# Optimization experiments

Measured on AMD Instinct MI355X. Metric: run time of the kernel, lower is better.

## Reference

```python
import jax, jax.numpy as jnp
import numpy as np

EMBED_DIM, NUM_HEADS, LOCAL_SIZE = 256, 4, 15
HEAD_DIM = EMBED_DIM // NUM_HEADS
SCALING = float(HEAD_DIM) ** -0.5


def get_overlap_segments(x, window_size):
    # x: (n, t, d) -> (n, t, window_size, d), zero-padded local windows centered at each position
    n, t, d = x.shape
    p = (window_size - 1) // 2
    xp = jnp.pad(x, ((0, 0), (p, p), (0, 0)))
    idx = jnp.arange(t)[:, None] + jnp.arange(window_size)[None, :]  # (t, w)
    return xp[:, idx]


def setup_inputs():
    key = jax.random.key(0)
    ks = jax.random.split(key, 4)
    B, W, F = 4, 64, 4096
    T = W + F
    x = jax.random.normal(ks[0], (B, T, EMBED_DIM), dtype=jnp.float32)
    # block one-hot frame->window assignment (each window owns F//W consecutive frames)
    assign = jnp.repeat(jnp.arange(W), F // W)
    wm = jnp.broadcast_to(jax.nn.one_hot(assign, W, dtype=jnp.float32).T[None], (B, W, F))
    W_qkv = jax.random.normal(ks[1], (EMBED_DIM, 3 * EMBED_DIM), jnp.float32) * 0.02
    b_qkv = jnp.zeros((3 * EMBED_DIM,), jnp.float32)
    W_out = jax.random.normal(ks[2], (EMBED_DIM, EMBED_DIM), jnp.float32) * 0.02
    b_out = jnp.zeros((EMBED_DIM,), jnp.float32)
    return {"x": x, "window_mapping": wm, "W_qkv": W_qkv, "b_qkv": b_qkv,
            "W_out": W_out, "b_out": b_out}


def _to_heads(z, b, t):
    # (b, t, E) -> (b*H, t, d), matching torch transpose/reshape ordering (b outer, h inner)
    return z.reshape(b, t, NUM_HEADS, HEAD_DIM).transpose(0, 2, 1, 3).reshape(b * NUM_HEADS, t, HEAD_DIM)


def reference(x, window_mapping, W_qkv, b_qkv, W_out, b_out):
    b, t, e = x.shape
    Wn, Fn = window_mapping.shape[1], window_mapping.shape[2]
    qkv = x @ W_qkv + b_qkv
    Q, K, V = jnp.split(qkv, 3, axis=-1)
    Q = Q * SCALING
    wtok = _to_heads(x[:, :Wn], b, Wn)            # (n, W, d) raw word tokens
    Qh = _to_heads(Q, b, t)[:, Wn:]               # (n, F, d)
    Kh = _to_heads(K, b, t)[:, Wn:]
    Vh = _to_heads(V, b, t)[:, Wn:]
    wm = jnp.broadcast_to(window_mapping[:, None], (b, NUM_HEADS, Wn, Fn)).reshape(b * NUM_HEADS, Wn, Fn)
    # scatter each window's word token to its frames
    expa = jnp.einsum('nwd,nwf->nfd', wtok, wm)   # (n, F, d)
    Kseg = get_overlap_segments(Kh, LOCAL_SIZE)   # (n, F, w, d)
    Vseg = get_overlap_segments(Vh, LOCAL_SIZE)
    Kcat = jnp.concatenate([expa[:, :, None], Kseg], axis=2)  # (n, F, 1+w, d)
    scores = jnp.einsum('nfd,nfwd->nfw', Qh, Kcat)            # (n, F, 1+w)
    # word-token weight: softmax across frames within each window chunk (F % W == 0, no pad)
    chunk = Fn // Wn
    w_wtok = jax.nn.softmax(scores[:, :, 0].reshape(-1, Wn, chunk), axis=-1).reshape(-1, Fn)
    # local-window weights: softmax over the window axis
    w_fea = jax.nn.softmax(scores[:, :, 1:], axis=-1)
    attn = jnp.concatenate([w_wtok[:, :, None], w_fea], axis=2)  # (n, F, 1+w)
    Vcat = jnp.concatenate([expa[:, :, None], Vseg], axis=2)
    out_fea = jnp.einsum('nfw,nfwd->nfd', attn, Vcat)            # (n, F, d)
    out = jnp.concatenate([wtok, out_fea], axis=1)               # (n, T, d)
    out = out.reshape(b, NUM_HEADS, t, HEAD_DIM).transpose(0, 2, 1, 3).reshape(b, t, e)
    return out @ W_out + b_out
```

## Files before the change

kernel.cpp:

```cpp
#include <hip/hip_runtime.h>


#define QN 4194304ull

typedef _Float16 h8 __attribute__((ext_vector_type(8)));
typedef _Float16 h4 __attribute__((ext_vector_type(4)));
typedef float f32x16 __attribute__((ext_vector_type(16)));

__global__ __launch_bounds__(256) void conv_small(
    const float* __restrict__ x, const float* __restrict__ wm,
    const float* __restrict__ Wq, const float* __restrict__ Wo,
    _Float16* __restrict__ wqth, _Float16* __restrict__ woth,
    _Float16* __restrict__ wmth, _Float16* __restrict__ xth) {
  __shared__ float S[64 * 65];
  const int g = blockIdx.x, tid = threadIdx.x;
  if (g < 768) {
    int o = g * 256 + tid;
    int n = o >> 8, k = o & 255;
    wqth[o] = (_Float16)Wq[(size_t)k * 768 + n];
  } else if (g < 1024) {
    int o = (g - 768) * 256 + tid;
    int n = o >> 8, k = o & 255;
    woth[o] = (_Float16)Wo[(size_t)k * 256 + n];
  } else if (g < 1280) {
    int local = g - 1024;
    int b = local >> 6, f0 = (local & 63) * 64;
    {
      int w = tid >> 2, c0 = (tid & 3) * 16;
      const float* src = wm + ((size_t)(b * 64 + w)) * 4096 + f0 + c0;
#pragma unroll
      for (int cc = 0; cc < 16; cc += 4)
        *(float4*)&S[w * 65 + c0 + cc] = *(const float4*)(src + cc);
    }
    __syncthreads();
    {
      int fl = tid >> 2, w0 = (tid & 3) * 16;
      int f = f0 + fl;
      _Float16 hh[16];
#pragma unroll
      for (int j = 0; j < 16; ++j) hh[j] = (_Float16)S[(w0 + j) * 65 + fl];
      size_t o = ((size_t)b * 4096 + f) * 64 + w0;
      *(float4*)(wmth + o) = *(float4*)&hh[0];
      *(float4*)(wmth + o + 8) = *(float4*)&hh[8];
    }
  } else {
    int b = g - 1280;
    for (int c0 = 0; c0 < 256; c0 += 64) {
      __syncthreads();
      {
        int w = tid >> 2, cl0 = (tid & 3) * 16;
        const float* src = x + ((size_t)(b * 4160 + w)) * 256 + c0 + cl0;
#pragma unroll
        for (int cc = 0; cc < 16; cc += 4)
          *(float4*)&S[w * 65 + cl0 + cc] = *(const float4*)(src + cc);
      }
      __syncthreads();
      {
        int cl = tid >> 2, w0 = (tid & 3) * 16;
        _Float16 hh[16];
#pragma unroll
        for (int j = 0; j < 16; ++j) hh[j] = (_Float16)S[(w0 + j) * 65 + cl];
        size_t o = ((size_t)(b * 256 + c0 + cl)) * 64 + w0;
        *(float4*)(xth + o) = *(float4*)&hh[0];
        *(float4*)(xth + o + 8) = *(float4*)&hh[8];
      }
    }
  }
}

__global__ __launch_bounds__(256) void qkv_mfma(
    const float* __restrict__ x, const _Float16* __restrict__ wth,
    const float* __restrict__ bq,
    _Float16* __restrict__ Qh, _Float16* __restrict__ Kh,
    _Float16* __restrict__ Vh) {
  __shared__ _Float16 Ah[128][40], Bh[128][40];
  const int tid = threadIdx.x;
  const int wave = tid >> 6, lane = tid & 63;
  const int ln = lane & 31, half = lane >> 5;
  const int mw = (wave & 1) * 64, nw = (wave >> 1) * 64;
  const int m0 = blockIdx.x * 128, n0 = blockIdx.y * 128;

  const int sr = tid >> 1, scq = (tid & 1) * 16;
  const int am = m0 + sr;
  const size_t arow =
      ((size_t)((am >> 12) * 4160 + 64 + (am & 4095))) * 256 + scq;
  const size_t brow = (size_t)(n0 + sr) * 256 + scq;

  float4 rah0, rah1, rbh0, rbh1;
  auto QLOAD = [&](int k0_) {
    float4 fx0 = *(const float4*)(x + arow + k0_);
    float4 fx1 = *(const float4*)(x + arow + k0_ + 4);
    float4 fx2 = *(const float4*)(x + arow + k0_ + 8);
    float4 fx3 = *(const float4*)(x + arow + k0_ + 12);
    rbh0 = *(const float4*)(wth + brow + k0_);
    rbh1 = *(const float4*)(wth + brow + k0_ + 8);
    _Float16 hh[16] = {
        (_Float16)fx0.x, (_Float16)fx0.y, (_Float16)fx0.z, (_Float16)fx0.w,
        (_Float16)fx1.x, (_Float16)fx1.y, (_Float16)fx1.z, (_Float16)fx1.w,
        (_Float16)fx2.x, (_Float16)fx2.y, (_Float16)fx2.z, (_Float16)fx2.w,
        (_Float16)fx3.x, (_Float16)fx3.y, (_Float16)fx3.z, (_Float16)fx3.w};
    rah0 = *(float4*)&hh[0];
    rah1 = *(float4*)&hh[8];
  };

  QLOAD(0);
  f32x16 acc[2][2] = {};

  for (int it = 0; it < 8; ++it) {
    __syncthreads();
    *(float4*)&Ah[sr][scq] = rah0;
    *(float4*)&Ah[sr][scq + 8] = rah1;
    *(float4*)&Bh[sr][scq] = rbh0;
    *(float4*)&Bh[sr][scq + 8] = rbh1;
    __syncthreads();
    if (it < 7) QLOAD((it + 1) * 32);
#pragma unroll
    for (int ks = 0; ks < 2; ++ks) {
      const int kc = ks * 16 + half * 8;
      h8 a0 = *(const h8*)&Ah[mw + ln][kc];
      h8 a1 = *(const h8*)&Ah[mw + 32 + ln][kc];
      h8 b0 = *(const h8*)&Bh[nw + ln][kc];
      h8 b1 = *(const h8*)&Bh[nw + 32 + ln][kc];
      acc[0][0] = __builtin_amdgcn_mfma_f32_32x32x16_f16(a0, b0, acc[0][0], 0, 0, 0);
      acc[0][1] = __builtin_amdgcn_mfma_f32_32x32x16_f16(a0, b1, acc[0][1], 0, 0, 0);
      acc[1][0] = __builtin_amdgcn_mfma_f32_32x32x16_f16(a1, b0, acc[1][0], 0, 0, 0);
      acc[1][1] = __builtin_amdgcn_mfma_f32_32x32x16_f16(a1, b1, acc[1][1], 0, 0, 0);
    }
  }

#pragma unroll
  for (int ni = 0; ni < 2; ++ni) {
    const int c = n0 + nw + ni * 32 + ln;
    const int which = c >> 8, e = c & 255;
    const int h = e >> 6, d = e & 63;
    _Float16* dst = (which == 0) ? Qh : (which == 1) ? Kh : Vh;
    const float sc2 = (which == 0) ? 0.125f : 1.0f;
    const float bias = bq[c];
#pragma unroll
    for (int mi = 0; mi < 2; ++mi) {
      const int rb = m0 + mw + mi * 32 + 4 * half;
#pragma unroll
      for (int reg = 0; reg < 16; ++reg) {
        int rr = rb + (reg & 3) + 8 * (reg >> 2);
        int b2 = rr >> 12, f2 = rr & 4095;
        dst[(((size_t)(b2 * 4 + h)) * 4096 + f2) * 64 + d] =
            (_Float16)((acc[mi][ni][reg] + bias) * sc2);
      }
    }
  }
}

__global__ __launch_bounds__(256) void attn_fused(
    const _Float16* __restrict__ Qh, const _Float16* __restrict__ Kh,
    const _Float16* __restrict__ Vh,
    const _Float16* __restrict__ wmth, const _Float16* __restrict__ xth,
    _Float16* __restrict__ OFh) {
  __shared__ float Ks[78][68];
  __shared__ float Vs[78][68];
  __shared__ float EXs[64][68];
  __shared__ float s0s[64];
  __shared__ float red[2];
  const int tid = threadIdx.x;
  const int w = blockIdx.x;
  const int n = blockIdx.y;
  const int f0 = w * 64;
  const int b = n >> 2, h = n & 3;

  for (int idx = tid; idx < 78 * 16; idx += 256) {
    int rr = idx >> 4, c = (idx & 15) * 4;
    int g = f0 - 7 + rr;
    float4 kv = {0.f, 0.f, 0.f, 0.f}, vv = {0.f, 0.f, 0.f, 0.f};
    if (g >= 0 && g < 4096) {
      size_t base = ((size_t)n * 4096 + g) * 64 + c;
      h4 k4 = *(const h4*)(Kh + base);
      h4 v4 = *(const h4*)(Vh + base);
      kv = {(float)k4.x, (float)k4.y, (float)k4.z, (float)k4.w};
      vv = {(float)v4.x, (float)v4.y, (float)v4.z, (float)v4.w};
    }
    *(float4*)&Ks[rr][c] = kv;
    *(float4*)&Vs[rr][c] = vv;
  }
  {
    const int wave = tid >> 6, lane = tid & 63;
    const int ln = lane & 31, half = lane >> 5;
    const int mi = wave & 1, ni = wave >> 1;
    const size_t arow = ((size_t)(b * 4096 + f0 + mi * 32 + ln)) * 64 + half * 8;
    const size_t brow =
        ((size_t)(b * 256 + h * 64 + ni * 32 + ln)) * 64 + half * 8;
    f32x16 eacc = {};
#pragma unroll
    for (int ks = 0; ks < 4; ++ks) {
      const int kc = ks * 16;
      h8 ah = *(const h8*)(wmth + arow + kc);
      h8 bh = *(const h8*)(xth + brow + kc);
      eacc = __builtin_amdgcn_mfma_f32_32x32x16_f16(ah, bh, eacc, 0, 0, 0);
    }
    const int col = ni * 32 + ln;
    const int rb2 = mi * 32 + 4 * half;
#pragma unroll
    for (int reg = 0; reg < 16; ++reg)
      EXs[rb2 + (reg & 3) + 8 * (reg >> 2)][col] = eacc[reg];
  }
  __syncthreads();

  const int i = tid >> 2, q = tid & 3;
  const int f = f0 + i;
  const size_t qbase = ((size_t)n * 4096 + f) * 64 + q * 16;
  h8 qh0 = *(const h8*)(Qh + qbase);
  h8 qh1 = *(const h8*)(Qh + qbase + 8);
  float4 q0 = {(float)qh0.s0, (float)qh0.s1, (float)qh0.s2, (float)qh0.s3};
  float4 q1 = {(float)qh0.s4, (float)qh0.s5, (float)qh0.s6, (float)qh0.s7};
  float4 q2 = {(float)qh1.s0, (float)qh1.s1, (float)qh1.s2, (float)qh1.s3};
  float4 q3 = {(float)qh1.s4, (float)qh1.s5, (float)qh1.s6, (float)qh1.s7};
  float4 e0 = *(const float4*)&EXs[i][q * 16];
  float4 e1 = *(const float4*)&EXs[i][q * 16 + 4];
  float4 e2 = *(const float4*)&EXs[i][q * 16 + 8];
  float4 e3 = *(const float4*)&EXs[i][q * 16 + 12];

  float s0 = q0.x * e0.x + q0.y * e0.y + q0.z * e0.z + q0.w * e0.w +
             q1.x * e1.x + q1.y * e1.y + q1.z * e1.z + q1.w * e1.w +
             q2.x * e2.x + q2.y * e2.y + q2.z * e2.z + q2.w * e2.w +
             q3.x * e3.x + q3.y * e3.y + q3.z * e3.z + q3.w * e3.w;
  s0 += __shfl_xor(s0, 1);
  s0 += __shfl_xor(s0, 2);

  float sj[15];
#pragma unroll
  for (int j = 0; j < 15; ++j) {
    const float* kr = &Ks[i + j][q * 16];
    float4 k0 = *(const float4*)(kr);
    float4 k1 = *(const float4*)(kr + 4);
    float4 k2 = *(const float4*)(kr + 8);
    float4 k3 = *(const float4*)(kr + 12);
    float s = q0.x * k0.x + q0.y * k0.y + q0.z * k0.z + q0.w * k0.w +
              q1.x * k1.x + q1.y * k1.y + q1.z * k1.z + q1.w * k1.w +
              q2.x * k2.x + q2.y * k2.y + q2.z * k2.z + q2.w * k2.w +
              q3.x * k3.x + q3.y * k3.y + q3.z * k3.z + q3.w * k3.w;
    s += __shfl_xor(s, 1);
    s += __shfl_xor(s, 2);
    sj[j] = s;
  }

  if (q == 0) s0s[i] = s0;
  __syncthreads();
  if (tid < 64) {
    float v = s0s[tid];
    float m = v;
    for (int o = 1; o < 64; o <<= 1) m = fmaxf(m, __shfl_xor(m, o));
    float ee = expf(v - m);
    float s = ee;
    for (int o = 1; o < 64; o <<= 1) s += __shfl_xor(s, o);
    if (tid == 0) { red[0] = m; red[1] = s; }
  }
  __syncthreads();
  const float wt = expf(s0 - red[0]) / red[1];

  float mx = sj[0];
#pragma unroll
  for (int j = 1; j < 15; ++j) mx = fmaxf(mx, sj[j]);
  float pj[15], den = 0.f;
#pragma unroll
  for (int j = 0; j < 15; ++j) { pj[j] = expf(sj[j] - mx); den += pj[j]; }
  const float inv = 1.0f / den;

  float o[16] = {wt * e0.x, wt * e0.y, wt * e0.z, wt * e0.w,
                 wt * e1.x, wt * e1.y, wt * e1.z, wt * e1.w,
                 wt * e2.x, wt * e2.y, wt * e2.z, wt * e2.w,
                 wt * e3.x, wt * e3.y, wt * e3.z, wt * e3.w};
#pragma unroll
  for (int j = 0; j < 15; ++j) {
    float wj = pj[j] * inv;
    const float* vr = &Vs[i + j][q * 16];
#pragma unroll
    for (int dd = 0; dd < 16; ++dd) o[dd] = fmaf(wj, vr[dd], o[dd]);
  }
  _Float16 oh[16];
#pragma unroll
  for (int dd = 0; dd < 16; ++dd) oh[dd] = (_Float16)o[dd];
  *(float4*)(OFh + qbase) = *(float4*)&oh[0];
  *(float4*)(OFh + qbase + 8) = *(float4*)&oh[8];
}

__global__ __launch_bounds__(256) void out_mfma(
    const float* __restrict__ x, const _Float16* __restrict__ ofh,
    const _Float16* __restrict__ wth, const float* __restrict__ bo,
    float* __restrict__ out) {
  __shared__ _Float16 Ah[64][72], Bh[64][72];
  const int tid = threadIdx.x;
  const int wave = tid >> 6, lane = tid & 63;
  const int ln = lane & 31, half = lane >> 5;
  const int mw = (wave & 1) * 32, nw = (wave >> 1) * 32;
  const int m0 = blockIdx.x * 64, n0 = blockIdx.y * 64;
  const int sr = tid >> 2, sc4 = (tid & 3) * 16;
  const int m = m0 + sr;
  const int b = m / 4160, tt = m % 4160;
  const bool useX = (tt < 64);
  const size_t xrow = ((size_t)(b * 4160 + tt)) * 256 + sc4;
  const long obase = ((long)(b * 4) * 4096 + (tt - 64)) * 64 + sc4;
  const size_t bbase = (size_t)(n0 + sr) * 256 + sc4;

  float4 ra0, ra1, rb0, rb1;
  auto OLOAD = [&](int k0_) {
    if (useX) {
      float4 fx0 = *(const float4*)(x + xrow + k0_);
      float4 fx1 = *(const float4*)(x + xrow + k0_ + 4);
      float4 fx2 = *(const float4*)(x + xrow + k0_ + 8);
      float4 fx3 = *(const float4*)(x + xrow + k0_ + 12);
      _Float16 hh[16] = {
          (_Float16)fx0.x, (_Float16)fx0.y, (_Float16)fx0.z, (_Float16)fx0.w,
          (_Float16)fx1.x, (_Float16)fx1.y, (_Float16)fx1.z, (_Float16)fx1.w,
          (_Float16)fx2.x, (_Float16)fx2.y, (_Float16)fx2.z, (_Float16)fx2.w,
          (_Float16)fx3.x, (_Float16)fx3.y, (_Float16)fx3.z, (_Float16)fx3.w};
      ra0 = *(float4*)&hh[0];
      ra1 = *(float4*)&hh[8];
    } else {
      size_t o_ = (size_t)(obase + (long)(k0_ >> 6) * 262144);
      ra0 = *(const float4*)(ofh + o_);
      ra1 = *(const float4*)(ofh + o_ + 8);
    }
    rb0 = *(const float4*)(wth + bbase + k0_);
    rb1 = *(const float4*)(wth + bbase + k0_ + 8);
  };

  OLOAD(0);
  f32x16 acc = {};
  for (int it = 0; it < 4; ++it) {
    __syncthreads();
    *(float4*)&Ah[sr][sc4] = ra0;
    *(float4*)&Ah[sr][sc4 + 8] = ra1;
    *(float4*)&Bh[sr][sc4] = rb0;
    *(float4*)&Bh[sr][sc4 + 8] = rb1;
    __syncthreads();
    if (it < 3) OLOAD((it + 1) * 64);
#pragma unroll
    for (int ks = 0; ks < 4; ++ks) {
      const int kc = ks * 16 + half * 8;
      h8 ah = *(const h8*)&Ah[mw + ln][kc];
      h8 bh = *(const h8*)&Bh[nw + ln][kc];
      acc = __builtin_amdgcn_mfma_f32_32x32x16_f16(ah, bh, acc, 0, 0, 0);
    }
  }
  const int c = n0 + nw + ln;
  const float bias = bo[c];
  const int rb = m0 + mw + 4 * half;
#pragma unroll
  for (int reg = 0; reg < 16; ++reg) {
    int rr = rb + (reg & 3) + 8 * (reg >> 2);
    out[(size_t)rr * 256 + c] = acc[reg] + bias;
  }
}

extern "C" void kernel_launch(void* const* d_in, const int* in_sizes, int n_in,
                              void* d_out, int out_size, void* d_ws, size_t ws_size,
                              hipStream_t stream) {
  const float* x  = (const float*)d_in[0];
  const float* wm = (const float*)d_in[1];
  const float* Wq = (const float*)d_in[2];
  const float* bq = (const float*)d_in[3];
  const float* Wo = (const float*)d_in[4];
  const float* bo = (const float*)d_in[5];
  float* out = (float*)d_out;

  _Float16* Qh   = (_Float16*)d_ws;
  _Float16* Kh   = Qh + QN;
  _Float16* Vh   = Kh + QN;
  _Float16* OFh  = Vh + QN;
  _Float16* Wqth = OFh + QN;
  _Float16* Woth = Wqth + 196608;
  _Float16* wmTh = Woth + 65536;
  _Float16* xTh  = wmTh + 1048576;

  conv_small<<<dim3(1284), 256, 0, stream>>>(x, wm, Wq, Wo, Wqth, Woth, wmTh,
                                             xTh);
  qkv_mfma<<<dim3(128, 6), 256, 0, stream>>>(x, Wqth, bq, Qh, Kh, Vh);
  attn_fused<<<dim3(64, 16), 256, 0, stream>>>(Qh, Kh, Vh, wmTh, xTh, OFh);
  out_mfma<<<dim3(260, 4), 256, 0, stream>>>(x, OFh, Woth, bo, out);
}
```

Before: 126.4 us.

## Pre-convert x to fp16 once and widen K/V staging loads, use fast exp

Adds a conversion pass in the prep kernel that writes x as fp16 once. The QKV GEMM and output GEMM then read half-width data instead of re-reading and converting fp32 x; QKV previously re-read x six times, once per N-block column. The attention kernel loads K/V with 8-wide fp16 vectors and uses __expf for the softmaxes. The cost is one extra full pass over x (read fp32, write fp16) and a larger prep grid, plus slightly less accurate exponentials.

```diff
diff --git a/kernel.cpp b/kernel.cpp
--- a/kernel.cpp
+++ b/kernel.cpp
@@ -11,7 +11,8 @@
     const float* __restrict__ x, const float* __restrict__ wm,
     const float* __restrict__ Wq, const float* __restrict__ Wo,
     _Float16* __restrict__ wqth, _Float16* __restrict__ woth,
-    _Float16* __restrict__ wmth, _Float16* __restrict__ xth) {
+    _Float16* __restrict__ wmth, _Float16* __restrict__ xth,
+    _Float16* __restrict__ xh) {
   __shared__ float S[64 * 65];
   const int g = blockIdx.x, tid = threadIdx.x;
   if (g < 768) {
@@ -43,7 +44,7 @@
       *(float4*)(wmth + o) = *(float4*)&hh[0];
       *(float4*)(wmth + o + 8) = *(float4*)&hh[8];
     }
-  } else {
+  } else if (g < 1284) {
     int b = g - 1280;
     for (int c0 = 0; c0 < 256; c0 += 64) {
       __syncthreads();
@@ -65,11 +66,19 @@
         *(float4*)(xth + o + 8) = *(float4*)&hh[8];
       }
     }
+  } else {
+    size_t base = (size_t)(g - 1284) * 4096 + (size_t)tid * 4;
+#pragma unroll
+    for (int c = 0; c < 4; ++c) {
+      float4 v = *(const float4*)(x + base + c * 1024);
+      h4 hv = {(_Float16)v.x, (_Float16)v.y, (_Float16)v.z, (_Float16)v.w};
+      *(h4*)(xh + base + c * 1024) = hv;
+    }
   }
 }
 
 __global__ __launch_bounds__(256) void qkv_mfma(
-    const float* __restrict__ x, const _Float16* __restrict__ wth,
+    const _Float16* __restrict__ xh, const _Float16* __restrict__ wth,
     const float* __restrict__ bq,
     _Float16* __restrict__ Qh, _Float16* __restrict__ Kh,
     _Float16* __restrict__ Vh) {
@@ -88,19 +97,10 @@
 
   float4 rah0, rah1, rbh0, rbh1;
   auto QLOAD = [&](int k0_) {
-    float4 fx0 = *(const float4*)(x + arow + k0_);
-    float4 fx1 = *(const float4*)(x + arow + k0_ + 4);
-    float4 fx2 = *(const float4*)(x + arow + k0_ + 8);
-    float4 fx3 = *(const float4*)(x + arow + k0_ + 12);
+    rah0 = *(const float4*)(xh + arow + k0_);
+    rah1 = *(const float4*)(xh + arow + k0_ + 8);
     rbh0 = *(const float4*)(wth + brow + k0_);
     rbh1 = *(const float4*)(wth + brow + k0_ + 8);
-    _Float16 hh[16] = {
-        (_Float16)fx0.x, (_Float16)fx0.y, (_Float16)fx0.z, (_Float16)fx0.w,
-        (_Float16)fx1.x, (_Float16)fx1.y, (_Float16)fx1.z, (_Float16)fx1.w,
-        (_Float16)fx2.x, (_Float16)fx2.y, (_Float16)fx2.z, (_Float16)fx2.w,
-        (_Float16)fx3.x, (_Float16)fx3.y, (_Float16)fx3.z, (_Float16)fx3.w};
-    rah0 = *(float4*)&hh[0];
-    rah1 = *(float4*)&hh[8];
   };
 
   QLOAD(0);
@@ -166,19 +166,23 @@
   const int f0 = w * 64;
   const int b = n >> 2, h = n & 3;
 
-  for (int idx = tid; idx < 78 * 16; idx += 256) {
-    int rr = idx >> 4, c = (idx & 15) * 4;
+  for (int idx = tid; idx < 78 * 8; idx += 256) {
+    int rr = idx >> 3, c = (idx & 7) * 8;
     int g = f0 - 7 + rr;
-    float4 kv = {0.f, 0.f, 0.f, 0.f}, vv = {0.f, 0.f, 0.f, 0.f};
+    float4 k0v = {0.f, 0.f, 0.f, 0.f}, k1v = k0v, v0v = k0v, v1v = k0v;
     if (g >= 0 && g < 4096) {
       size_t base = ((size_t)n * 4096 + g) * 64 + c;
-      h4 k4 = *(const h4*)(Kh + base);
-      h4 v4 = *(const h4*)(Vh + base);
-      kv = {(float)k4.x, (float)k4.y, (float)k4.z, (float)k4.w};
-      vv = {(float)v4.x, (float)v4.y, (float)v4.z, (float)v4.w};
-    }
-    *(float4*)&Ks[rr][c] = kv;
-    *(float4*)&Vs[rr][c] = vv;
+      h8 k8 = *(const h8*)(Kh + base);
+      h8 v8 = *(const h8*)(Vh + base);
+      k0v = {(float)k8.s0, (float)k8.s1, (float)k8.s2, (float)k8.s3};
+      k1v = {(float)k8.s4, (float)k8.s5, (float)k8.s6, (float)k8.s7};
+      v0v = {(float)v8.s0, (float)v8.s1, (float)v8.s2, (float)v8.s3};
+      v1v = {(float)v8.s4, (float)v8.s5, (float)v8.s6, (float)v8.s7};
+    }
+    *(float4*)&Ks[rr][c] = k0v;
+    *(float4*)&Ks[rr][c + 4] = k1v;
+    *(float4*)&Vs[rr][c] = v0v;
+    *(float4*)&Vs[rr][c + 4] = v1v;
   }
   {
     const int wave = tid >> 6, lane = tid & 63;
@@ -247,20 +251,20 @@
     float v = s0s[tid];
     float m = v;
     for (int o = 1; o < 64; o <<= 1) m = fmaxf(m, __shfl_xor(m, o));
-    float ee = expf(v - m);
+    float ee = __expf(v - m);
     float s = ee;
     for (int o = 1; o < 64; o <<= 1) s += __shfl_xor(s, o);
     if (tid == 0) { red[0] = m; red[1] = s; }
   }
   __syncthreads();
-  const float wt = expf(s0 - red[0]) / red[1];
+  const float wt = __expf(s0 - red[0]) / red[1];
 
   float mx = sj[0];
 #pragma unroll
   for (int j = 1; j < 15; ++j) mx = fmaxf(mx, sj[j]);
   float pj[15], den = 0.f;
 #pragma unroll
-  for (int j = 0; j < 15; ++j) { pj[j] = expf(sj[j] - mx); den += pj[j]; }
+  for (int j = 0; j < 15; ++j) { pj[j] = __expf(sj[j] - mx); den += pj[j]; }
   const float inv = 1.0f / den;
 
   float o[16] = {wt * e0.x, wt * e0.y, wt * e0.z, wt * e0.w,
@@ -282,7 +286,7 @@
 }
 
 __global__ __launch_bounds__(256) void out_mfma(
-    const float* __restrict__ x, const _Float16* __restrict__ ofh,
+    const _Float16* __restrict__ xh, const _Float16* __restrict__ ofh,
     const _Float16* __restrict__ wth, const float* __restrict__ bo,
     float* __restrict__ out) {
   __shared__ _Float16 Ah[64][72], Bh[64][72];
@@ -302,17 +306,8 @@
   float4 ra0, ra1, rb0, rb1;
   auto OLOAD = [&](int k0_) {
     if (useX) {
-      float4 fx0 = *(const float4*)(x + xrow + k0_);
-      float4 fx1 = *(const float4*)(x + xrow + k0_ + 4);
-      float4 fx2 = *(const float4*)(x + xrow + k0_ + 8);
-      float4 fx3 = *(const float4*)(x + xrow + k0_ + 12);
-      _Float16 hh[16] = {
-          (_Float16)fx0.x, (_Float16)fx0.y, (_Float16)fx0.z, (_Float16)fx0.w,
-          (_Float16)fx1.x, (_Float16)fx1.y, (_Float16)fx1.z, (_Float16)fx1.w,
-          (_Float16)fx2.x, (_Float16)fx2.y, (_Float16)fx2.z, (_Float16)fx2.w,
-          (_Float16)fx3.x, (_Float16)fx3.y, (_Float16)fx3.z, (_Float16)fx3.w};
-      ra0 = *(float4*)&hh[0];
-      ra1 = *(float4*)&hh[8];
+      ra0 = *(const float4*)(xh + xrow + k0_);
+      ra1 = *(const float4*)(xh + xrow + k0_ + 8);
     } else {
       size_t o_ = (size_t)(obase + (long)(k0_ >> 6) * 262144);
       ra0 = *(const float4*)(ofh + o_);
@@ -369,10 +364,11 @@
   _Float16* Woth = Wqth + 196608;
   _Float16* wmTh = Woth + 65536;
   _Float16* xTh  = wmTh + 1048576;
-
-  conv_small<<<dim3(1284), 256, 0, stream>>>(x, wm, Wq, Wo, Wqth, Woth, wmTh,
-                                             xTh);
-  qkv_mfma<<<dim3(128, 6), 256, 0, stream>>>(x, Wqth, bq, Qh, Kh, Vh);
+  _Float16* xh   = xTh + 65536;
+
+  conv_small<<<dim3(2324), 256, 0, stream>>>(x, wm, Wq, Wo, Wqth, Woth, wmTh,
+                                             xTh, xh);
+  qkv_mfma<<<dim3(128, 6), 256, 0, stream>>>(xh, Wqth, bq, Qh, Kh, Vh);
   attn_fused<<<dim3(64, 16), 256, 0, stream>>>(Qh, Kh, Vh, wmTh, xTh, OFh);
-  out_mfma<<<dim3(260, 4), 256, 0, stream>>>(x, OFh, Woth, bo, out);
-}
+  out_mfma<<<dim3(260, 4), 256, 0, stream>>>(xh, OFh, Woth, bo, out);
+}
```

Result: faster. 121.1 us (-4.2%).
